# Kernel optimization log

Measured on AMD Instinct MI355X. Metric: run time of the kernel, lower is better.

The kernel has to match this reference:

```python
import jax, jax.numpy as jnp
import numpy as np


def _dsepconv(inp, vertical, horizontal, offset_x, offset_y, mask):
    # inp: [B,C,H,W]; vertical/horizontal: [B,F,H,W]; offset_x/offset_y/mask: [B,F*F,H,W]
    B, C, H, W = inp.shape
    F_ = min(vertical.shape[1], horizontal.shape[1])
    T = F_ * F_
    out_h = min(vertical.shape[2], horizontal.shape[2])
    out_w = min(vertical.shape[3], horizontal.shape[3])

    fy = jnp.repeat(jnp.arange(F_), F_).astype(inp.dtype)   # [T] tap row index
    fx = jnp.tile(jnp.arange(F_), F_).astype(inp.dtype)     # [T] tap col index
    h_idx = jnp.arange(out_h, dtype=inp.dtype)
    w_idx = jnp.arange(out_w, dtype=inp.dtype)
    c_off = (F_ - 1) / 2.0

    # NOTE: original code uses offset_y for the x coordinate and offset_x for y (faithful swap)
    x_norm = 2.0 * (offset_y + w_idx[None, None, None, :] + fx[None, :, None, None] - c_off + 1.0) / W - 1.0
    y_norm = 2.0 * (offset_x + h_idx[None, None, :, None] + fy[None, :, None, None] - c_off + 1.0) / H - 1.0
    x_norm = jnp.clip(x_norm, -1.0, 1.0)
    y_norm = jnp.clip(y_norm, -1.0, 1.0)

    # grid_sample align_corners=False mapping to pixel coords
    ix = ((x_norm + 1.0) * W - 1.0) / 2.0   # [B,T,H,W]
    iy = ((y_norm + 1.0) * H - 1.0) / 2.0

    x0 = jnp.floor(ix)
    y0 = jnp.floor(iy)
    wx1 = ix - x0  # fractional weights
    wy1 = iy - y0
    wx0 = 1.0 - wx1
    wy0 = 1.0 - wy1

    # border padding: clamp integer neighbor indices
    x0i = jnp.clip(x0.astype(jnp.int32), 0, W - 1)
    x1i = jnp.clip(x0.astype(jnp.int32) + 1, 0, W - 1)
    y0i = jnp.clip(y0.astype(jnp.int32), 0, H - 1)
    y1i = jnp.clip(y0.astype(jnp.int32) + 1, 0, H - 1)

    def gather(img, yi, xi):  # img [C,H,W], yi/xi [T,h,w] -> [C,T,h,w]
        return img[:, yi, xi]
    g = jax.vmap(gather)  # over batch -> [B,C,T,h,w]

    # combined per-tap coefficient: vertical[fy] * horizontal[fx] * mask[tap]
    coef = (vertical[:, jnp.repeat(jnp.arange(F_), F_), :out_h, :out_w]
            * horizontal[:, jnp.tile(jnp.arange(F_), F_), :out_h, :out_w]
            * mask[:, :, :out_h, :out_w])  # [B,T,h,w]

    out = (jnp.einsum('bthw,bcthw->bchw', coef * wy0 * wx0, g(inp, y0i, x0i))
           + jnp.einsum('bthw,bcthw->bchw', coef * wy0 * wx1, g(inp, y0i, x1i))
           + jnp.einsum('bthw,bcthw->bchw', coef * wy1 * wx0, g(inp, y1i, x0i))
           + jnp.einsum('bthw,bcthw->bchw', coef * wy1 * wx1, g(inp, y1i, x1i)))
    return out


def setup_inputs() -> dict:
    key = jax.random.key(0)
    k = jax.random.split(key, 6)
    B, C, H, W, F_ = 2, 3, 512, 512, 5
    T = F_ * F_
    return {
        'tensorInput': jax.random.normal(k[0], (B, C, H, W), dtype=jnp.float32),
        'tensorVertical': jax.random.uniform(k[1], (B, F_, H, W), dtype=jnp.float32),
        'tensorHorizontal': jax.random.uniform(k[2], (B, F_, H, W), dtype=jnp.float32),
        'tensorOffsetX': jax.random.normal(k[3], (B, T, H, W), dtype=jnp.float32),
        'tensorOffsetY': jax.random.normal(k[4], (B, T, H, W), dtype=jnp.float32),
        'tensorMask': jax.random.uniform(k[5], (B, T, H, W), dtype=jnp.float32),
    }


def reference(tensorInput, tensorVertical, tensorHorizontal, tensorOffsetX, tensorOffsetY, tensorMask):
    return _dsepconv(tensorInput, tensorVertical, tensorHorizontal, tensorOffsetX, tensorOffsetY, tensorMask)
```

## Files before the change

kernel.cpp:

```cpp
#include <hip/hip_runtime.h>

#define B_ 2
#define C_ 3
#define H_ 512
#define W_ 512
#define F_ 5
#define T_ 25
#define HW_ (H_ * W_)
#define PW_ 520
#define PH_ 513

#define TBW 64
#define TBH 4
#define RY  10
#define RX  10
#define TRH (TBH + 2 * RY + 1)
#define TCW 89
#define TILE_N (TRH * TCW)

#define NT(p) __builtin_nontemporal_load(p)

typedef _Float16 h4 __attribute__((ext_vector_type(4), aligned(8)));

__global__ __launch_bounds__(256) void repack_kernel(
    const float* __restrict__ inp, h4* __restrict__ pk)
{
    const int x   = (blockIdx.x << 8) + threadIdx.x;
    const int row = blockIdx.y;
    const int b   = blockIdx.z;
    const int sr  = row < H_ ? row : H_ - 1;
    const float* p = inp + b * (C_ * HW_) + (sr << 9) + x;
    h4 v;
    v.x = (_Float16)p[0];
    v.y = (_Float16)p[HW_];
    v.z = (_Float16)p[2 * HW_];
    v.w = (_Float16)0.f;
    h4* dst = pk + b * (PH_ * PW_) + row * PW_;
    dst[x] = v;
    if (x == W_ - 1) dst[W_] = v;
}

__global__ __launch_bounds__(256) void dsepconv_kernel(
    const h4* __restrict__ pk,
    const float* __restrict__ vert,
    const float* __restrict__ horz,
    const float* __restrict__ offx,
    const float* __restrict__ offy,
    const float* __restrict__ mask,
    float* __restrict__ out)
{
    __shared__ h4 tile[TILE_N];

    const int tid  = threadIdx.x;
    const int lane = tid & 63;
    const int wv   = tid >> 6;
    const int h0   = blockIdx.y * TBH;
    const int w0b  = blockIdx.x * TBW;
    const int b    = blockIdx.z;
    const int h    = h0 + wv;
    const int w    = w0b + lane;

    const int hw = (h << 9) | w;

    const float* vb   = vert + b * (F_ * HW_) + hw;
    const float* hb   = horz + b * (F_ * HW_) + hw;
    const float* ob_x = offx + b * (T_ * HW_) + hw;
    const float* ob_y = offy + b * (T_ * HW_) + hw;
    const float* mb   = mask + b * (T_ * HW_) + hw;
    const h4* pb      = pk + b * (PH_ * PW_);

    float hz[F_];
#pragma unroll
    for (int f = 0; f < F_; ++f) hz[f] = NT(hb + f * HW_);

    float cy[F_], cx[F_], cm[F_];
#pragma unroll
    for (int fx = 0; fx < F_; ++fx) {
        cy[fx] = NT(ob_y + fx * HW_);
        cx[fx] = NT(ob_x + fx * HW_);
        cm[fx] = NT(mb   + fx * HW_);
    }

    {
        const int colg0 = w0b - RX + lane;
        const int gc0 = min(max(colg0, 0), W_);
        const int gc1 = min(max(colg0 + 64, 0), W_);
#pragma unroll
        for (int r0 = 0; r0 < 7; ++r0) {
            const int r = r0 * 4 + wv;
            if (r < TRH) {
                const int gr = min(max(h0 - RY + r, 0), H_);
                const h4* src = pb + gr * PW_;
                tile[r * TCW + lane] = src[gc0];
                if (lane < TCW - 64)
                    tile[r * TCW + 64 + lane] = src[gc1];
            }
        }
    }
    __syncthreads();

    float acc0 = 0.f, acc1 = 0.f, acc2 = 0.f;

    const float xbase = (float)(lane + RX) - 1.5f;
    const float ybase = (float)(wv + RY) - 1.5f;
    const float xlo = -0.5f - (float)(w0b - RX);
    const float xhi = ((float)W_ - 0.5f) - (float)(w0b - RX);
    const float ylo = -0.5f - (float)(h0 - RY);
    const float yhi = ((float)H_ - 0.5f) - (float)(h0 - RY);

#pragma unroll 1
    for (int fy = 0; fy < F_; ++fy) {
        float ny[F_], nx2[F_], nm[F_];
        if (fy + 1 < F_) {
            const int nb = (fy + 1) * F_;
#pragma unroll
            for (int fx = 0; fx < F_; ++fx) {
                ny[fx]  = NT(ob_y + (nb + fx) * HW_);
                nx2[fx] = NT(ob_x + (nb + fx) * HW_);
                nm[fx]  = NT(mb   + (nb + fx) * HW_);
            }
        }

        const float vfy = NT(vb + fy * HW_);
        const float yb  = ybase + (float)fy;

#pragma unroll
        for (int fx = 0; fx < F_; ++fx) {
            const float oy = cy[fx];
            const float ox = cx[fx];
            const float m  = cm[fx];

            float ixf = oy + (xbase + (float)fx);
            float iyf = ox + yb;
            ixf = fminf(fmaxf(ixf, xlo), xhi);
            iyf = fminf(fmaxf(iyf, ylo), yhi);

            float x0f = floorf(ixf), y0f = floorf(iyf);
            float wx1 = (ixf - x0f);
            float wy1 = (iyf - y0f);
            wx1 = (x0f < xlo) ? 0.f : wx1;
            wy1 = (y0f < ylo) ? 0.f : wy1;

            const int tc = min(max((int)x0f, 0), TCW - 2);
            const int ty = min(max((int)y0f, 0), TRH - 2);

            const h4* p = &tile[ty * TCW + tc];
            const h4 t00 = p[0];
            const h4 t01 = p[1];
            const h4 t10 = p[TCW];
            const h4 t11 = p[TCW + 1];

            const _Float16 wx1h = (_Float16)wx1;
            const _Float16 wx0h = (_Float16)1.f - wx1h;
            const _Float16 wy1h = (_Float16)wy1;
            const _Float16 wy0h = (_Float16)1.f - wy1h;
            const h4 wx0v = { wx0h, wx0h, wx0h, wx0h };
            const h4 wx1v = { wx1h, wx1h, wx1h, wx1h };
            const h4 wy0v = { wy0h, wy0h, wy0h, wy0h };
            const h4 wy1v = { wy1h, wy1h, wy1h, wy1h };

            const h4 rt = t00 * wx0v + t01 * wx1v;
            const h4 rb = t10 * wx0v + t11 * wx1v;
            const h4 r  = rt * wy0v + rb * wy1v;

            const float coef = vfy * hz[fx] * m;
            acc0 += coef * (float)r.x;
            acc1 += coef * (float)r.y;
            acc2 += coef * (float)r.z;
        }

        if (fy + 1 < F_) {
#pragma unroll
            for (int fx = 0; fx < F_; ++fx) {
                cy[fx] = ny[fx];
                cx[fx] = nx2[fx];
                cm[fx] = nm[fx];
            }
        }
    }

    float* ob = out + b * (C_ * HW_) + hw;
    __builtin_nontemporal_store(acc0, ob);
    __builtin_nontemporal_store(acc1, ob + HW_);
    __builtin_nontemporal_store(acc2, ob + 2 * HW_);
}

extern "C" void kernel_launch(void* const* d_in, const int* in_sizes, int n_in,
                              void* d_out, int out_size, void* d_ws, size_t ws_size,
                              hipStream_t stream) {
    const float* inp  = (const float*)d_in[0];
    const float* vert = (const float*)d_in[1];
    const float* horz = (const float*)d_in[2];
    const float* offx = (const float*)d_in[3];
    const float* offy = (const float*)d_in[4];
    const float* mask = (const float*)d_in[5];
    float* out = (float*)d_out;
    h4* pk = (h4*)d_ws;

    dim3 blockR(256), gridR(W_ / 256, PH_, B_);
    hipLaunchKernelGGL(repack_kernel, gridR, blockR, 0, stream, inp, pk);

    dim3 block(256);
    dim3 grid(W_ / TBW, H_ / TBH, B_);
    hipLaunchKernelGGL(dsepconv_kernel, grid, block, 0, stream,
                       pk, vert, horz, offx, offy, mask, out);
}
```

Measured before the change: 187.3 us.

## Process two output rows per thread with taller tile and drop nontemporal loads

```diff
diff --git a/kernel.cpp b/kernel.cpp
--- a/kernel.cpp
+++ b/kernel.cpp
@@ -11,14 +11,12 @@
 #define PH_ 513
 
 #define TBW 64
-#define TBH 4
+#define TBH 8
 #define RY  10
 #define RX  10
 #define TRH (TBH + 2 * RY + 1)
 #define TCW 89
 #define TILE_N (TRH * TCW)
-
-#define NT(p) __builtin_nontemporal_load(p)
 
 typedef _Float16 h4 __attribute__((ext_vector_type(4), aligned(8)));
 
@@ -40,7 +38,7 @@
     if (x == W_ - 1) dst[W_] = v;
 }
 
-__global__ __launch_bounds__(256) void dsepconv_kernel(
+__global__ __launch_bounds__(256, 4) void dsepconv_kernel(
     const h4* __restrict__ pk,
     const float* __restrict__ vert,
     const float* __restrict__ horz,
@@ -57,28 +55,32 @@
     const int h0   = blockIdx.y * TBH;
     const int w0b  = blockIdx.x * TBW;
     const int b    = blockIdx.z;
-    const int h    = h0 + wv;
     const int w    = w0b + lane;
 
-    const int hw = (h << 9) | w;
-
-    const float* vb   = vert + b * (F_ * HW_) + hw;
-    const float* hb   = horz + b * (F_ * HW_) + hw;
-    const float* ob_x = offx + b * (T_ * HW_) + hw;
-    const float* ob_y = offy + b * (T_ * HW_) + hw;
-    const float* mb   = mask + b * (T_ * HW_) + hw;
+    const int hwA = ((h0 + wv) << 9) | w;
+    const int hwB = hwA + (4 << 9);
+
+    const float* vbA  = vert + b * (F_ * HW_) + hwA;
+    const float* vbB  = vert + b * (F_ * HW_) + hwB;
+    const float* hbA  = horz + b * (F_ * HW_) + hwA;
+    const float* hbB  = horz + b * (F_ * HW_) + hwB;
+    const float* oxA  = offx + b * (T_ * HW_) + hwA;
+    const float* oxB  = offx + b * (T_ * HW_) + hwB;
+    const float* oyA  = offy + b * (T_ * HW_) + hwA;
+    const float* oyB  = offy + b * (T_ * HW_) + hwB;
+    const float* mbA  = mask + b * (T_ * HW_) + hwA;
+    const float* mbB  = mask + b * (T_ * HW_) + hwB;
     const h4* pb      = pk + b * (PH_ * PW_);
 
-    float hz[F_];
-#pragma unroll
-    for (int f = 0; f < F_; ++f) hz[f] = NT(hb + f * HW_);
-
-    float cy[F_], cx[F_], cm[F_];
+    float hzA[F_], hzB[F_];
+#pragma unroll
+    for (int f = 0; f < F_; ++f) { hzA[f] = hbA[f * HW_]; hzB[f] = hbB[f * HW_]; }
+
+    float cyA[F_], cxA[F_], cmA[F_], cyB[F_], cxB[F_], cmB[F_];
 #pragma unroll
     for (int fx = 0; fx < F_; ++fx) {
-        cy[fx] = NT(ob_y + fx * HW_);
-        cx[fx] = NT(ob_x + fx * HW_);
-        cm[fx] = NT(mb   + fx * HW_);
+        cyA[fx] = oyA[fx * HW_];  cxA[fx] = oxA[fx * HW_];  cmA[fx] = mbA[fx * HW_];
+        cyB[fx] = oyB[fx * HW_];  cxB[fx] = oxB[fx * HW_];  cmB[fx] = mbB[fx * HW_];
     }
 
     {
@@ -86,7 +88,7 @@
         const int gc0 = min(max(colg0, 0), W_);
         const int gc1 = min(max(colg0 + 64, 0), W_);
 #pragma unroll
-        for (int r0 = 0; r0 < 7; ++r0) {
+        for (int r0 = 0; r0 < 8; ++r0) {
             const int r = r0 * 4 + wv;
             if (r < TRH) {
                 const int gr = min(max(h0 - RY + r, 0), H_);
@@ -99,10 +101,12 @@
     }
     __syncthreads();
 
-    float acc0 = 0.f, acc1 = 0.f, acc2 = 0.f;
-
-    const float xbase = (float)(lane + RX) - 1.5f;
-    const float ybase = (float)(wv + RY) - 1.5f;
+    float aA0 = 0.f, aA1 = 0.f, aA2 = 0.f;
+    float aB0 = 0.f, aB1 = 0.f, aB2 = 0.f;
+
+    const float xbase  = (float)(lane + RX) - 1.5f;
+    const float ybaseA = (float)(wv + RY) - 1.5f;
+    const float ybaseB = ybaseA + 4.f;
     const float xlo = -0.5f - (float)(w0b - RX);
     const float xhi = ((float)W_ - 0.5f) - (float)(w0b - RX);
     const float ylo = -0.5f - (float)(h0 - RY);
@@ -110,79 +114,104 @@
 
 #pragma unroll 1
     for (int fy = 0; fy < F_; ++fy) {
-        float ny[F_], nx2[F_], nm[F_];
+        float nyA[F_], nxA[F_], nmA[F_], nyB[F_], nxB[F_], nmB[F_];
         if (fy + 1 < F_) {
             const int nb = (fy + 1) * F_;
 #pragma unroll
             for (int fx = 0; fx < F_; ++fx) {
-                ny[fx]  = NT(ob_y + (nb + fx) * HW_);
-                nx2[fx] = NT(ob_x + (nb + fx) * HW_);
-                nm[fx]  = NT(mb   + (nb + fx) * HW_);
-            }
-        }
-
-        const float vfy = NT(vb + fy * HW_);
-        const float yb  = ybase + (float)fy;
+                nyA[fx] = oyA[(nb + fx) * HW_];
+                nxA[fx] = oxA[(nb + fx) * HW_];
+                nmA[fx] = mbA[(nb + fx) * HW_];
+                nyB[fx] = oyB[(nb + fx) * HW_];
+                nxB[fx] = oxB[(nb + fx) * HW_];
+                nmB[fx] = mbB[(nb + fx) * HW_];
+            }
+        }
+
+        const float vfyA = vbA[fy * HW_];
+        const float vfyB = vbB[fy * HW_];
+        const float ybA  = ybaseA + (float)fy;
+        const float ybB  = ybaseB + (float)fy;
 
 #pragma unroll
         for (int fx = 0; fx < F_; ++fx) {
-            const float oy = cy[fx];
-            const float ox = cx[fx];
-            const float m  = cm[fx];
-
-            float ixf = oy + (xbase + (float)fx);
-            float iyf = ox + yb;
-            ixf = fminf(fmaxf(ixf, xlo), xhi);
-            iyf = fminf(fmaxf(iyf, ylo), yhi);
-
-            float x0f = floorf(ixf), y0f = floorf(iyf);
-            float wx1 = (ixf - x0f);
-            float wy1 = (iyf - y0f);
-            wx1 = (x0f < xlo) ? 0.f : wx1;
-            wy1 = (y0f < ylo) ? 0.f : wy1;
-
-            const int tc = min(max((int)x0f, 0), TCW - 2);
-            const int ty = min(max((int)y0f, 0), TRH - 2);
-
-            const h4* p = &tile[ty * TCW + tc];
-            const h4 t00 = p[0];
-            const h4 t01 = p[1];
-            const h4 t10 = p[TCW];
-            const h4 t11 = p[TCW + 1];
-
-            const _Float16 wx1h = (_Float16)wx1;
-            const _Float16 wx0h = (_Float16)1.f - wx1h;
-            const _Float16 wy1h = (_Float16)wy1;
-            const _Float16 wy0h = (_Float16)1.f - wy1h;
-            const h4 wx0v = { wx0h, wx0h, wx0h, wx0h };
-            const h4 wx1v = { wx1h, wx1h, wx1h, wx1h };
-            const h4 wy0v = { wy0h, wy0h, wy0h, wy0h };
-            const h4 wy1v = { wy1h, wy1h, wy1h, wy1h };
-
-            const h4 rt = t00 * wx0v + t01 * wx1v;
-            const h4 rb = t10 * wx0v + t11 * wx1v;
-            const h4 r  = rt * wy0v + rb * wy1v;
-
-            const float coef = vfy * hz[fx] * m;
-            acc0 += coef * (float)r.x;
-            acc1 += coef * (float)r.y;
-            acc2 += coef * (float)r.z;
+            {
+                float ixf = cyA[fx] + (xbase + (float)fx);
+                float iyf = cxA[fx] + ybA;
+                ixf = fminf(fmaxf(ixf, xlo), xhi);
+                iyf = fminf(fmaxf(iyf, ylo), yhi);
+                float x0f = floorf(ixf), y0f = floorf(iyf);
+                float wx1 = ixf - x0f, wy1 = iyf - y0f;
+                wx1 = (x0f < xlo) ? 0.f : wx1;
+                wy1 = (y0f < ylo) ? 0.f : wy1;
+                const int tc = min(max((int)x0f, 0), TCW - 2);
+                const int ty = min(max((int)y0f, 0), TRH - 2);
+                const h4* p = &tile[ty * TCW + tc];
+                const h4 t00 = p[0], t01 = p[1], t10 = p[TCW], t11 = p[TCW + 1];
+                const _Float16 wx1h = (_Float16)wx1;
+                const _Float16 wx0h = (_Float16)1.f - wx1h;
+                const _Float16 wy1h = (_Float16)wy1;
+                const _Float16 wy0h = (_Float16)1.f - wy1h;
+                const h4 wx0v = { wx0h, wx0h, wx0h, wx0h };
+                const h4 wx1v = { wx1h, wx1h, wx1h, wx1h };
+                const h4 wy0v = { wy0h, wy0h, wy0h, wy0h };
+                const h4 wy1v = { wy1h, wy1h, wy1h, wy1h };
+                const h4 rt = t00 * wx0v + t01 * wx1v;
+                const h4 rb = t10 * wx0v + t11 * wx1v;
+                const h4 r  = rt * wy0v + rb * wy1v;
+                const float coef = vfyA * hzA[fx] * cmA[fx];
+                aA0 += coef * (float)r.x;
+                aA1 += coef * (float)r.y;
+                aA2 += coef * (float)r.z;
+            }
+            {
+                float ixf = cyB[fx] + (xbase + (float)fx);
+                float iyf = cxB[fx] + ybB;
+                ixf = fminf(fmaxf(ixf, xlo), xhi);
+                iyf = fminf(fmaxf(iyf, ylo), yhi);
+                float x0f = floorf(ixf), y0f = floorf(iyf);
+                float wx1 = ixf - x0f, wy1 = iyf - y0f;
+                wx1 = (x0f < xlo) ? 0.f : wx1;
+                wy1 = (y0f < ylo) ? 0.f : wy1;
+                const int tc = min(max((int)x0f, 0), TCW - 2);
+                const int ty = min(max((int)y0f, 0), TRH - 2);
+                const h4* p = &tile[ty * TCW + tc];
+                const h4 t00 = p[0], t01 = p[1], t10 = p[TCW], t11 = p[TCW + 1];
+                const _Float16 wx1h = (_Float16)wx1;
+                const _Float16 wx0h = (_Float16)1.f - wx1h;
+                const _Float16 wy1h = (_Float16)wy1;
+                const _Float16 wy0h = (_Float16)1.f - wy1h;
+                const h4 wx0v = { wx0h, wx0h, wx0h, wx0h };
+                const h4 wx1v = { wx1h, wx1h, wx1h, wx1h };
+                const h4 wy0v = { wy0h, wy0h, wy0h, wy0h };
+                const h4 wy1v = { wy1h, wy1h, wy1h, wy1h };
+                const h4 rt = t00 * wx0v + t01 * wx1v;
+                const h4 rb = t10 * wx0v + t11 * wx1v;
+                const h4 r  = rt * wy0v + rb * wy1v;
+                const float coef = vfyB * hzB[fx] * cmB[fx];
+                aB0 += coef * (float)r.x;
+                aB1 += coef * (float)r.y;
+                aB2 += coef * (float)r.z;
+            }
         }
 
         if (fy + 1 < F_) {
 #pragma unroll
             for (int fx = 0; fx < F_; ++fx) {
-                cy[fx] = ny[fx];
-                cx[fx] = nx2[fx];
-                cm[fx] = nm[fx];
+                cyA[fx] = nyA[fx]; cxA[fx] = nxA[fx]; cmA[fx] = nmA[fx];
+                cyB[fx] = nyB[fx]; cxB[fx] = nxB[fx]; cmB[fx] = nmB[fx];
             }
         }
     }
 
-    float* ob = out + b * (C_ * HW_) + hw;
-    __builtin_nontemporal_store(acc0, ob);
-    __builtin_nontemporal_store(acc1, ob + HW_);
-    __builtin_nontemporal_store(acc2, ob + 2 * HW_);
+    float* obA = out + b * (C_ * HW_) + hwA;
+    float* obB = out + b * (C_ * HW_) + hwB;
+    __builtin_nontemporal_store(aA0, obA);
+    __builtin_nontemporal_store(aA1, obA + HW_);
+    __builtin_nontemporal_store(aA2, obA + 2 * HW_);
+    __builtin_nontemporal_store(aB0, obB);
+    __builtin_nontemporal_store(aB1, obB + HW_);
+    __builtin_nontemporal_store(aB2, obB + 2 * HW_);
 }
 
 extern "C" void kernel_launch(void* const* d_in, const int* in_sizes, int n_in,
```

Result: slower. 445.0 us (+137.6%).
